# Performance work log

Hardware: AMD Instinct MI355X
Metric: run time of the kernel (lower is better)

The kernel has to match this reference:

```python
import jax, jax.numpy as jnp
import numpy as np
import math

B, N_AGENT, E = 32, 64, 256        # batch, agents, n_embd
DV, NV, HIS, DK = 32, 8, 50, 9     # head dim, heads, his_length, action_dim+1


def positional_encoding(max_seq_len, d_model):
    position = jnp.arange(max_seq_len, dtype=jnp.float32)[:, None]
    div_term = jnp.exp(jnp.arange(0, d_model, 2, dtype=jnp.float32) * (-math.log(10000.0) / d_model))
    pe = jnp.zeros((max_seq_len, d_model), jnp.float32)
    pe = pe.at[:, 0::2].set(jnp.sin(position * div_term))
    pe = pe.at[:, 1::2].set(jnp.cos(position * div_term))
    return pe


def setup_inputs() -> dict:
    key = jax.random.key(0)
    ks = jax.random.split(key, 12)
    q = jax.random.normal(ks[0], (B, N_AGENT, E), jnp.float32)
    k = jax.random.normal(ks[1], (B, HIS, N_AGENT, DK), jnp.float32)
    # adjacency: one-hot row selecting, per (agent, timestep), which agent's action to gather
    idx = jax.random.randint(ks[2], (N_AGENT, HIS), 0, N_AGENT)
    adjs_pos = jax.nn.one_hot(idx, N_AGENT, dtype=jnp.float32)  # [N, HIS, N]
    s = 0.05
    return {
        "q": q,
        "k": k,
        "adjs_pos": adjs_pos,
        "Wq": s * jax.random.normal(ks[3], (E, DV * NV), jnp.float32),
        "bq": jnp.zeros((DV * NV,), jnp.float32),
        "Wk": s * jax.random.normal(ks[4], (E, DV * NV), jnp.float32),
        "bk": jnp.zeros((DV * NV,), jnp.float32),
        "Wv": s * jax.random.normal(ks[5], (E, DV * NV), jnp.float32),
        "bv": jnp.zeros((DV * NV,), jnp.float32),
        "Wout": s * jax.random.normal(ks[6], (DV * NV, E), jnp.float32),
        "bout": jnp.zeros((E,), jnp.float32),
        "Wenc": s * jax.random.normal(ks[7], (DK, E), jnp.float32),
    }


def reference(q, k, adjs_pos, Wq, bq, Wk, bk, Wv, bv, Wout, bout, Wenc):
    b, n, e = q.shape
    d_k = k.shape[-1]  # torch code scales by sqrt(k.size(-1)) = 9
    pe = positional_encoding(HIS, e)  # [HIS, E]

    # query head: relu(Linear) then split heads -> [B, N, NV, DV]
    qh = jax.nn.relu(q @ Wq + bq).reshape(b, n, NV, DV)

    # adjacency gather: one-hot matmul selecting a neighbor's action per (agent, t)
    # avoids materializing the repeated [B,N,HIS,N,DK] tensor
    neigh = jnp.einsum('ntA,btAd->bntd', adjs_pos, k)  # [B, N, HIS, DK]

    # action encoder (GELU, exact erf as in nn.GELU) + positional encoding
    neigh = jax.nn.gelu(neigh @ Wenc, approximate=False) + pe  # [B, N, HIS, E]

    # key/value heads
    kh = jax.nn.relu(neigh @ Wk + bk).reshape(b, n, HIS, NV, DV)
    vh = jax.nn.relu(neigh @ Wv + bv).reshape(b, n, HIS, NV, DV)

    # attention over the history axis
    att = jnp.einsum('bnvd,bntvd->bnvt', qh, kh) / jnp.sqrt(jnp.float32(d_k))
    att = jax.nn.softmax(att, axis=-1)  # [B, N, NV, HIS]

    out = jnp.einsum('bnvt,bntvd->bnvd', att, vh).reshape(b, n, NV * DV)
    return jax.nn.relu(out @ Wout + bout)  # [B, N, E]
```

## Files before the change

### kernel.cpp

```cpp
#include <hip/hip_runtime.h>
#include <math.h>

#define NB   32
#define NA   64
#define EDIM 256
#define HIS  50
#define DKA  9
#define NV   8

typedef _Float16 HALF;
typedef _Float16 half4 __attribute__((ext_vector_type(4)));
typedef _Float16 half8 __attribute__((ext_vector_type(8)));
typedef float    f32x4 __attribute__((ext_vector_type(4)));

#define WS_WKP   0
#define WS_WVP   131072
#define WS_WQP   262144
#define WS_WOP   393216
#define WS_PEH   524288
#define WS_WET   549888
#define WS_IDX   566272
#define WS_QH    579072
#define WS_NEED  1627648ULL

__device__ __forceinline__ float gelu_exact(float x) {
    const float ax = fabsf(x) * 0.70710678118654752f;
    const float t  = __builtin_amdgcn_rcpf(1.0f + 0.3275911f * ax);
    const float p  = t * (0.254829592f + t * (-0.284496736f + t * (1.421413741f
                   + t * (-1.453152027f + t * 1.061405429f))));
    const float er = 1.0f - p * __expf(-ax * ax);
    return 0.5f * x * (1.0f + copysignf(er, x));
}

__global__ __launch_bounds__(256) void pack_setup(
    const float* __restrict__ Wk, const float* __restrict__ Wv,
    const float* __restrict__ Wq, const float* __restrict__ Wout,
    const float* __restrict__ adjs, const float* __restrict__ Wenc,
    char* __restrict__ ws)
{
    const int tid = blockIdx.x * 256 + threadIdx.x;
    HALF* WkP  = (HALF*)(ws + WS_WKP);
    HALF* WvP  = (HALF*)(ws + WS_WVP);
    HALF* WqP  = (HALF*)(ws + WS_WQP);
    HALF* WoP  = (HALF*)(ws + WS_WOP);
    HALF* PEH  = (HALF*)(ws + WS_PEH);
    HALF* WET  = (HALF*)(ws + WS_WET);
    int*  idxT = (int*)(ws + WS_IDX);

    {
        const int elem = tid & 7;
        const int lane = (tid >> 3) & 63;
        const int kt   = (tid >> 9) & 7;
        const int nt   = tid >> 12;
        const int k = kt * 32 + (lane >> 4) * 8 + elem;
        const int n = nt * 16 + (lane & 15);
        WkP[tid] = (HALF)Wk[k * EDIM + n];
        WvP[tid] = (HALF)Wv[k * EDIM + n];
        WqP[tid] = (HALF)Wq[k * EDIM + n];
        WoP[tid] = (HALF)Wout[k * EDIM + n];
    }
    if (tid < HIS * EDIM) {
        const int t = tid >> 8;
        const int e = tid & 255;
        const float dt = expf(-(float)(e & ~1) * (9.210340371976184f / 256.0f));
        const float arg = (float)t * dt;
        PEH[tid] = (HALF)((e & 1) ? cosf(arg) : sinf(arg));
    }
    if (tid < 16 * 64 * 8) {
        const int j    = tid & 7;
        const int lane = (tid >> 3) & 63;
        const int me   = tid >> 9;
        const int k = (lane >> 4) * 8 + j;
        const int e = me * 16 + (lane & 15);
        WET[tid] = (k < DKA) ? (HALF)Wenc[k * EDIM + e] : (HALF)0.0f;
    }
    if (tid < NA * HIS) {
        const float* row = adjs + tid * NA;
        int best = 0;
        #pragma unroll
        for (int a = 0; a < NA; ++a) best = (row[a] > 0.5f) ? a : best;
        idxT[tid] = best;
    }
}

__global__ __launch_bounds__(256) void qh_gemm(
    const float* __restrict__ q,
    const float* __restrict__ bq,
    const char*  __restrict__ ws,
    char* __restrict__ wsout)
{
    const int tid = threadIdx.x, lane = tid & 63, w = tid >> 6;
    const int l15 = lane & 15, l4 = lane >> 4;
    const int bx  = blockIdx.x;
    const int r0  = (bx >> 1) * 64;
    const int nh  = bx & 1;
    const HALF* WqP = (const HALF*)(ws + WS_WQP);
    HALF* qh = (HALF*)(wsout + WS_QH);

    f32x4 acc[4][2];
    #pragma unroll
    for (int mt = 0; mt < 4; ++mt)
        #pragma unroll
        for (int nt = 0; nt < 2; ++nt) acc[mt][nt] = (f32x4)0.0f;

    #pragma unroll 2
    for (int kk = 0; kk < 8; ++kk) {
        half8 afr[4];
        #pragma unroll
        for (int mt = 0; mt < 4; ++mt) {
            const float* ap = &q[(size_t)(r0 + mt * 16 + l15) * EDIM + kk * 32 + l4 * 8];
            const float4 a0 = *reinterpret_cast<const float4*>(ap);
            const float4 a1 = *reinterpret_cast<const float4*>(ap + 4);
            half8 h;
            h[0] = (HALF)a0.x; h[1] = (HALF)a0.y; h[2] = (HALF)a0.z; h[3] = (HALF)a0.w;
            h[4] = (HALF)a1.x; h[5] = (HALF)a1.y; h[6] = (HALF)a1.z; h[7] = (HALF)a1.w;
            afr[mt] = h;
        }
        #pragma unroll
        for (int nt = 0; nt < 2; ++nt) {
            const int ntile = nh * 8 + w * 2 + nt;
            const half8 bfr = *reinterpret_cast<const half8*>(
                WqP + ((size_t)(ntile * 8 + kk) * 64 + lane) * 8);
            #pragma unroll
            for (int mt = 0; mt < 4; ++mt)
                acc[mt][nt] = __builtin_amdgcn_mfma_f32_16x16x32_f16(afr[mt], bfr, acc[mt][nt], 0, 0, 0);
        }
    }

    #pragma unroll
    for (int nt = 0; nt < 2; ++nt) {
        const int col = (nh * 8 + w * 2 + nt) * 16 + l15;
        const float bqa = bq[col];
        #pragma unroll
        for (int mt = 0; mt < 4; ++mt)
            #pragma unroll
            for (int r = 0; r < 4; ++r) {
                const int row = l4 * 4 + r;
                qh[(size_t)(r0 + mt * 16 + row) * EDIM + col] =
                    (HALF)fmaxf(acc[mt][nt][r] + bqa, 0.0f);
            }
    }
}

__global__ __launch_bounds__(512, 4) void attn_fused(
    const float* __restrict__ kin,
    const float* __restrict__ bk,
    const float* __restrict__ bv,
    const char*  __restrict__ ws,
    char* __restrict__ wsout)
{
    const int tid  = threadIdx.x;
    const int lane = tid & 63;
    const int w    = tid >> 6;
    const int l15  = lane & 15;
    const int l4   = lane >> 4;
    const int bidx = blockIdx.x;
    const int b = bidx >> 6, n = bidx & 63;

    const HALF* WkP  = (const HALF*)(ws + WS_WKP);
    const HALF* WvP  = (const HALF*)(ws + WS_WVP);
    const HALF* PEH  = (const HALF*)(ws + WS_PEH);
    const HALF* WET  = (const HALF*)(ws + WS_WET);
    const HALF* qh   = (const HALF*)(ws + WS_QH);
    const int*  idxT = (const int*)(ws + WS_IDX);
    HALF* O = (HALF*)(wsout + WS_QH);

    __shared__ __align__(16) HALF  s_A[16384];
    __shared__ __align__(16) float s_un[1280];
    __shared__ float s_att[NV][64];

    HALF*  s_ng = (HALF*)s_un;
    float* s_o  = s_un;

    float qv[2], bkb[2], bvb[2];
    #pragma unroll
    for (int nt = 0; nt < 2; ++nt) {
        const int col = w * 32 + nt * 16 + l15;
        qv[nt]  = (float)qh[(size_t)bidx * EDIM + col];
        bkb[nt] = bk[col];
        bvb[nt] = bv[col];
    }

    #pragma unroll
    for (int i0 = 0; i0 < 64 * 32; i0 += 512) {
        const int i = i0 + tid;
        const int t = i >> 5;
        const int d = i & 31;
        float v = 0.0f;
        if (t < HIS && d < DKA)
            v = kin[((b * HIS + t) * NA + idxT[n * HIS + t]) * DKA + d];
        s_ng[t * 40 + d] = (HALF)v;
    }
    __syncthreads();

    {
        half8 aW[2];
        #pragma unroll
        for (int mi = 0; mi < 2; ++mi)
            aW[mi] = *reinterpret_cast<const half8*>(WET + ((size_t)(2 * w + mi) * 64 + lane) * 8);

        f32x4 accE[2][4];
        #pragma unroll
        for (int mi = 0; mi < 2; ++mi)
            #pragma unroll
            for (int nt = 0; nt < 4; ++nt) accE[mi][nt] = (f32x4)0.0f;

        #pragma unroll
        for (int nt = 0; nt < 4; ++nt) {
            const half8 bN = *reinterpret_cast<const half8*>(&s_ng[(nt * 16 + l15) * 40 + l4 * 8]);
            #pragma unroll
            for (int mi = 0; mi < 2; ++mi)
                accE[mi][nt] = __builtin_amdgcn_mfma_f32_16x16x32_f16(aW[mi], bN, accE[mi][nt], 0, 0, 0);
        }

        const int t_l = l4 & 1;
        #pragma unroll
        for (int mi = 0; mi < 2; ++mi) {
            const int me = 2 * w + mi;
            const int e0 = me * 16 + l4 * 4;
            const int fg = mi * 2 + (l4 >> 1);
            #pragma unroll
            for (int nt = 0; nt < 4; ++nt) {
                const int t = nt * 16 + l15;
                half4 hv;
                if (t < HIS) {
                    const half4 pe = *reinterpret_cast<const half4*>(PEH + t * EDIM + e0);
                    hv[0] = (HALF)(gelu_exact(accE[mi][nt][0]) + (float)pe[0]);
                    hv[1] = (HALF)(gelu_exact(accE[mi][nt][1]) + (float)pe[1]);
                    hv[2] = (HALF)(gelu_exact(accE[mi][nt][2]) + (float)pe[2]);
                    hv[3] = (HALF)(gelu_exact(accE[mi][nt][3]) + (float)pe[3]);
                } else {
                    hv[0] = (HALF)0.0f; hv[1] = (HALF)0.0f;
                    hv[2] = (HALF)0.0f; hv[3] = (HALF)0.0f;
                }
                const int gran = (w * 4 + nt) * 64 + ((fg * 16 + l15) ^ w);
                *reinterpret_cast<half4*>(&s_A[gran * 8 + t_l * 4]) = hv;
            }
        }
    }
    __syncthreads();

    f32x4 ka[4][2], va[4][2];
    #pragma unroll
    for (int mt = 0; mt < 4; ++mt)
        #pragma unroll
        for (int nt = 0; nt < 2; ++nt) { ka[mt][nt] = (f32x4)0.0f; va[mt][nt] = (f32x4)0.0f; }

    #pragma unroll
    for (int kk = 0; kk < 8; ++kk) {
        half8 afr[4];
        #pragma unroll
        for (int mt = 0; mt < 4; ++mt)
            afr[mt] = *reinterpret_cast<const half8*>(
                &s_A[((kk * 4 + mt) * 64 + (lane ^ kk)) * 8]);
        #pragma unroll
        for (int nt = 0; nt < 2; ++nt) {
            const size_t boff = ((size_t)((w * 2 + nt) * 8 + kk) * 64 + lane) * 8;
            const half8 bkfr = *reinterpret_cast<const half8*>(WkP + boff);
            const half8 bvfr = *reinterpret_cast<const half8*>(WvP + boff);
            #pragma unroll
            for (int mt = 0; mt < 4; ++mt) {
                ka[mt][nt] = __builtin_amdgcn_mfma_f32_16x16x32_f16(afr[mt], bkfr, ka[mt][nt], 0, 0, 0);
                va[mt][nt] = __builtin_amdgcn_mfma_f32_16x16x32_f16(afr[mt], bvfr, va[mt][nt], 0, 0, 0);
            }
        }
    }

    #pragma unroll
    for (int mt = 0; mt < 4; ++mt)
        #pragma unroll
        for (int r = 0; r < 4; ++r) {
            float p = qv[0] * fmaxf(ka[mt][0][r] + bkb[0], 0.0f)
                    + qv[1] * fmaxf(ka[mt][1][r] + bkb[1], 0.0f);
            p += __shfl_xor(p, 1);
            p += __shfl_xor(p, 2);
            p += __shfl_xor(p, 4);
            p += __shfl_xor(p, 8);
            if (l15 == 0) s_att[w][mt * 16 + l4 * 4 + r] = p * (1.0f / 3.0f);
        }

    {
        const float val = (lane < HIS) ? s_att[w][lane] : -1e30f;
        float m = val;
        m = fmaxf(m, __shfl_xor(m, 1));
        m = fmaxf(m, __shfl_xor(m, 2));
        m = fmaxf(m, __shfl_xor(m, 4));
        m = fmaxf(m, __shfl_xor(m, 8));
        m = fmaxf(m, __shfl_xor(m, 16));
        m = fmaxf(m, __shfl_xor(m, 32));
        const float e = (lane < HIS) ? __expf(val - m) : 0.0f;
        float s = e;
        s += __shfl_xor(s, 1);
        s += __shfl_xor(s, 2);
        s += __shfl_xor(s, 4);
        s += __shfl_xor(s, 8);
        s += __shfl_xor(s, 16);
        s += __shfl_xor(s, 32);
        s_att[w][lane] = e * __builtin_amdgcn_rcpf(s);
    }

    {
        float o0 = 0.f, o1 = 0.f;
        #pragma unroll
        for (int mt = 0; mt < 4; ++mt)
            #pragma unroll
            for (int r = 0; r < 4; ++r) {
                const int t = mt * 16 + l4 * 4 + r;
                const float a = s_att[w][t];
                o0 += a * fmaxf(va[mt][0][r] + bvb[0], 0.0f);
                o1 += a * fmaxf(va[mt][1][r] + bvb[1], 0.0f);
            }
        o0 += __shfl_xor(o0, 16); o1 += __shfl_xor(o1, 16);
        o0 += __shfl_xor(o0, 32); o1 += __shfl_xor(o1, 32);
        __syncthreads();
        if (lane < 16) {
            s_o[w * 32 +  0 + l15] = o0;
            s_o[w * 32 + 16 + l15] = o1;
        }
    }
    __syncthreads();

    if (tid < 256) O[(size_t)bidx * EDIM + tid] = (HALF)s_o[tid];
}

__global__ __launch_bounds__(256) void out_gemm(
    const float* __restrict__ bout,
    const char*  __restrict__ ws,
    float* __restrict__ out)
{
    const int tid = threadIdx.x, lane = tid & 63, w = tid >> 6;
    const int l15 = lane & 15, l4 = lane >> 4;
    const int bx  = blockIdx.x;
    const int r0  = (bx >> 1) * 64;
    const int nh  = bx & 1;
    const HALF* WoP = (const HALF*)(ws + WS_WOP);
    const HALF* O   = (const HALF*)(ws + WS_QH);

    f32x4 acc[4][2];
    #pragma unroll
    for (int mt = 0; mt < 4; ++mt)
        #pragma unroll
        for (int nt = 0; nt < 2; ++nt) acc[mt][nt] = (f32x4)0.0f;

    #pragma unroll 2
    for (int kk = 0; kk < 8; ++kk) {
        half8 afr[4];
        #pragma unroll
        for (int mt = 0; mt < 4; ++mt)
            afr[mt] = *reinterpret_cast<const half8*>(
                &O[(size_t)(r0 + mt * 16 + l15) * EDIM + kk * 32 + l4 * 8]);
        #pragma unroll
        for (int nt = 0; nt < 2; ++nt) {
            const int ntile = nh * 8 + w * 2 + nt;
            const half8 bfr = *reinterpret_cast<const half8*>(
                WoP + ((size_t)(ntile * 8 + kk) * 64 + lane) * 8);
            #pragma unroll
            for (int mt = 0; mt < 4; ++mt)
                acc[mt][nt] = __builtin_amdgcn_mfma_f32_16x16x32_f16(afr[mt], bfr, acc[mt][nt], 0, 0, 0);
        }
    }

    #pragma unroll
    for (int nt = 0; nt < 2; ++nt) {
        const int col = (nh * 8 + w * 2 + nt) * 16 + l15;
        const float boa = bout[col];
        #pragma unroll
        for (int mt = 0; mt < 4; ++mt)
            #pragma unroll
            for (int r = 0; r < 4; ++r) {
                const int row = l4 * 4 + r;
                out[(size_t)(r0 + mt * 16 + row) * EDIM + col] =
                    fmaxf(acc[mt][nt][r] + boa, 0.0f);
            }
    }
}

__global__ __launch_bounds__(256) void mha_fallback(
    const float* __restrict__ q,
    const float* __restrict__ kin,
    const float* __restrict__ adjs,
    const float* __restrict__ Wq, const float* __restrict__ bq,
    const float* __restrict__ Wk, const float* __restrict__ bk,
    const float* __restrict__ Wv, const float* __restrict__ bv,
    const float* __restrict__ Wout, const float* __restrict__ bout,
    const float* __restrict__ Wenc,
    float* __restrict__ out)
{
    const int tid  = threadIdx.x;
    const int bidx = blockIdx.x;
    const int b = bidx >> 6;
    const int n = bidx & 63;

    __shared__ __align__(16) float s_q[EDIM];
    __shared__ __align__(16) float s_qh[EDIM];
    __shared__ __align__(16) float s_neigh[HIS][12];
    __shared__ __align__(16) float s_enc[HIS * EDIM];
    __shared__ float s_att[NV][66];
    __shared__ __align__(16) float s_opart[4][EDIM];
    __shared__ __align__(16) float s_o[EDIM];
    __shared__ int s_idx[HIS];

    s_q[tid] = q[bidx * EDIM + tid];
    if (tid < HIS) {
        const float* row = adjs + (n * HIS + tid) * NA;
        int best = 0;
        #pragma unroll
        for (int a = 0; a < NA; ++a) best = (row[a] > 0.5f) ? a : best;
        s_idx[tid] = best;
    }
    __syncthreads();

    for (int i = tid; i < HIS * 12; i += 256) {
        const int t = i / 12;
        const int d = i - t * 12;
        float val = 0.0f;
        if (d < DKA) val = kin[((b * HIS + t) * NA + s_idx[t]) * DKA + d];
        s_neigh[t][d] = val;
    }
    __syncthreads();

    {
        const int e = tid;
        float acc = bq[e];
        #pragma unroll 4
        for (int d0 = 0; d0 < EDIM; d0 += 4) {
            const float4 qv = *reinterpret_cast<const float4*>(&s_q[d0]);
            acc += qv.x * Wq[(d0 + 0) * EDIM + e];
            acc += qv.y * Wq[(d0 + 1) * EDIM + e];
            acc += qv.z * Wq[(d0 + 2) * EDIM + e];
            acc += qv.w * Wq[(d0 + 3) * EDIM + e];
        }
        s_qh[e] = fmaxf(acc, 0.0f);

        float we[12];
        #pragma unroll
        for (int j = 0; j < 12; ++j) we[j] = (j < DKA) ? Wenc[j * EDIM + e] : 0.0f;
        const float dt = expf(-(float)(e & ~1) * (9.210340371976184f / 256.0f));
        for (int t = 0; t < HIS; ++t) {
            const float4 n0 = *reinterpret_cast<const float4*>(&s_neigh[t][0]);
            const float4 n1 = *reinterpret_cast<const float4*>(&s_neigh[t][4]);
            const float4 n2 = *reinterpret_cast<const float4*>(&s_neigh[t][8]);
            float x = n0.x*we[0] + n0.y*we[1] + n0.z*we[2] + n0.w*we[3]
                    + n1.x*we[4] + n1.y*we[5] + n1.z*we[6] + n1.w*we[7]
                    + n2.x*we[8];
            x = 0.5f * x * (1.0f + erff(x * 0.70710678118654752f));
            const float arg = (float)t * dt;
            const float pe = (e & 1) ? cosf(arg) : sinf(arg);
            s_enc[t * EDIM + e] = x + pe;
        }
    }
    __syncthreads();

    const int g = tid & 63;
    const int h = tid >> 6;
    const int tbase  = (h == 0) ? 0 : (h == 1) ? 13 : (h == 2) ? 25 : 37;
    const int tcount = (h == 1 || h == 2) ? 12 : 13;
    const int v = g >> 3;

    {
        float4 kacc[13];
        const float4 bkv = *reinterpret_cast<const float4*>(&bk[4 * g]);
        #pragma unroll
        for (int tt = 0; tt < 13; ++tt) kacc[tt] = bkv;
        #pragma unroll 2
        for (int d0 = 0; d0 < EDIM; d0 += 4) {
            const float4 w0 = *reinterpret_cast<const float4*>(&Wk[(d0 + 0) * EDIM + 4 * g]);
            const float4 w1 = *reinterpret_cast<const float4*>(&Wk[(d0 + 1) * EDIM + 4 * g]);
            const float4 w2 = *reinterpret_cast<const float4*>(&Wk[(d0 + 2) * EDIM + 4 * g]);
            const float4 w3 = *reinterpret_cast<const float4*>(&Wk[(d0 + 3) * EDIM + 4 * g]);
            #pragma unroll
            for (int tt = 0; tt < 13; ++tt) {
                const float4 ev = *reinterpret_cast<const float4*>(&s_enc[(tbase + tt) * EDIM + d0]);
                kacc[tt].x += ev.x * w0.x + ev.y * w1.x + ev.z * w2.x + ev.w * w3.x;
                kacc[tt].y += ev.x * w0.y + ev.y * w1.y + ev.z * w2.y + ev.w * w3.y;
                kacc[tt].z += ev.x * w0.z + ev.y * w1.z + ev.z * w2.z + ev.w * w3.z;
                kacc[tt].w += ev.x * w0.w + ev.y * w1.w + ev.z * w2.w + ev.w * w3.w;
            }
        }
        const float4 qv = *reinterpret_cast<const float4*>(&s_qh[4 * g]);
        #pragma unroll
        for (int tt = 0; tt < 13; ++tt) {
            float p = qv.x * fmaxf(kacc[tt].x, 0.0f)
                    + qv.y * fmaxf(kacc[tt].y, 0.0f)
                    + qv.z * fmaxf(kacc[tt].z, 0.0f)
                    + qv.w * fmaxf(kacc[tt].w, 0.0f);
            p += __shfl_xor(p, 1);
            p += __shfl_xor(p, 2);
            p += __shfl_xor(p, 4);
            if ((g & 7) == 0) s_att[v][tbase + tt] = p * (1.0f / 3.0f);
        }
    }
    __syncthreads();

    if (tid < NV) {
        float m = -1e30f;
        for (int t = 0; t < HIS; ++t) m = fmaxf(m, s_att[tid][t]);
        float ssum = 0.0f;
        for (int t = 0; t < HIS; ++t) {
            const float ex = expf(s_att[tid][t] - m);
            s_att[tid][t] = ex;
            ssum += ex;
        }
        const float inv = 1.0f / ssum;
        for (int t = 0; t < HIS; ++t) s_att[tid][t] *= inv;
    }
    __syncthreads();

    {
        float4 vacc[13];
        const float4 bvv = *reinterpret_cast<const float4*>(&bv[4 * g]);
        #pragma unroll
        for (int tt = 0; tt < 13; ++tt) vacc[tt] = bvv;
        #pragma unroll 2
        for (int d0 = 0; d0 < EDIM; d0 += 4) {
            const float4 w0 = *reinterpret_cast<const float4*>(&Wv[(d0 + 0) * EDIM + 4 * g]);
            const float4 w1 = *reinterpret_cast<const float4*>(&Wv[(d0 + 1) * EDIM + 4 * g]);
            const float4 w2 = *reinterpret_cast<const float4*>(&Wv[(d0 + 2) * EDIM + 4 * g]);
            const float4 w3 = *reinterpret_cast<const float4*>(&Wv[(d0 + 3) * EDIM + 4 * g]);
            #pragma unroll
            for (int tt = 0; tt < 13; ++tt) {
                const float4 ev = *reinterpret_cast<const float4*>(&s_enc[(tbase + tt) * EDIM + d0]);
                vacc[tt].x += ev.x * w0.x + ev.y * w1.x + ev.z * w2.x + ev.w * w3.x;
                vacc[tt].y += ev.x * w0.y + ev.y * w1.y + ev.z * w2.y + ev.w * w3.y;
                vacc[tt].z += ev.x * w0.z + ev.y * w1.z + ev.z * w2.z + ev.w * w3.z;
                vacc[tt].w += ev.x * w0.w + ev.y * w1.w + ev.z * w2.w + ev.w * w3.w;
            }
        }
        float4 po = make_float4(0.0f, 0.0f, 0.0f, 0.0f);
        #pragma unroll
        for (int tt = 0; tt < 13; ++tt) {
            if (tt < tcount) {
                const float a = s_att[v][tbase + tt];
                po.x += a * fmaxf(vacc[tt].x, 0.0f);
                po.y += a * fmaxf(vacc[tt].y, 0.0f);
                po.z += a * fmaxf(vacc[tt].z, 0.0f);
                po.w += a * fmaxf(vacc[tt].w, 0.0f);
            }
        }
        *reinterpret_cast<float4*>(&s_opart[h][4 * g]) = po;
    }
    __syncthreads();

    s_o[tid] = s_opart[0][tid] + s_opart[1][tid] + s_opart[2][tid] + s_opart[3][tid];
    __syncthreads();

    {
        const int e = tid;
        float acc = bout[e];
        #pragma unroll 4
        for (int d0 = 0; d0 < EDIM; d0 += 4) {
            const float4 ov = *reinterpret_cast<const float4*>(&s_o[d0]);
            acc += ov.x * Wout[(d0 + 0) * EDIM + e];
            acc += ov.y * Wout[(d0 + 1) * EDIM + e];
            acc += ov.z * Wout[(d0 + 2) * EDIM + e];
            acc += ov.w * Wout[(d0 + 3) * EDIM + e];
        }
        out[bidx * EDIM + e] = fmaxf(acc, 0.0f);
    }
}

extern "C" void kernel_launch(void* const* d_in, const int* in_sizes, int n_in,
                              void* d_out, int out_size, void* d_ws, size_t ws_size,
                              hipStream_t stream) {
    const float* q    = (const float*)d_in[0];
    const float* kin  = (const float*)d_in[1];
    const float* adjs = (const float*)d_in[2];
    const float* Wq   = (const float*)d_in[3];
    const float* bq   = (const float*)d_in[4];
    const float* Wk   = (const float*)d_in[5];
    const float* bk   = (const float*)d_in[6];
    const float* Wv   = (const float*)d_in[7];
    const float* bv   = (const float*)d_in[8];
    const float* Wout = (const float*)d_in[9];
    const float* bout = (const float*)d_in[10];
    const float* Wenc = (const float*)d_in[11];
    float* out = (float*)d_out;
    char* ws = (char*)d_ws;

    if (ws_size >= WS_NEED) {
        hipLaunchKernelGGL(pack_setup, dim3(256), dim3(256), 0, stream,
                           Wk, Wv, Wq, Wout, adjs, Wenc, ws);
        hipLaunchKernelGGL(qh_gemm, dim3(64), dim3(256), 0, stream,
                           q, bq, ws, ws);
        hipLaunchKernelGGL(attn_fused, dim3(NB * NA), dim3(512), 0, stream,
                           kin, bk, bv, ws, ws);
        hipLaunchKernelGGL(out_gemm, dim3(64), dim3(256), 0, stream,
                           bout, ws, out);
    } else {
        hipLaunchKernelGGL(mha_fallback, dim3(NB * NA), dim3(256), 0, stream,
                           q, kin, adjs, Wq, bq, Wk, bk, Wv, bv, Wout, bout, Wenc, out);
    }
}
```

Measured before the change: 82.60 us.

## Split K and V projections across waves, two rows per block

The attention kernel now handles two (batch, agent) rows per block with 1024 threads. Waves 0-7 compute the K projection and waves 8-15 compute the V projection, each over both rows, so every weight fragment loaded from global memory is reused for two rows. The Q and output GEMMs halve their row tile to 32 and double the grid to 128 blocks for better CU coverage. In exchange, shared memory per block doubles, block-wide syncs are added between the score, softmax and output phases, and occupancy may be limited by the 1024-thread blocks.

```diff
diff --git a/kernel.cpp b/kernel.cpp
--- a/kernel.cpp
+++ b/kernel.cpp
@@ -92,22 +92,22 @@
     const int tid = threadIdx.x, lane = tid & 63, w = tid >> 6;
     const int l15 = lane & 15, l4 = lane >> 4;
     const int bx  = blockIdx.x;
-    const int r0  = (bx >> 1) * 64;
+    const int r0  = (bx >> 1) * 32;
     const int nh  = bx & 1;
     const HALF* WqP = (const HALF*)(ws + WS_WQP);
     HALF* qh = (HALF*)(wsout + WS_QH);
 
-    f32x4 acc[4][2];
-    #pragma unroll
-    for (int mt = 0; mt < 4; ++mt)
+    f32x4 acc[2][2];
+    #pragma unroll
+    for (int mt = 0; mt < 2; ++mt)
         #pragma unroll
         for (int nt = 0; nt < 2; ++nt) acc[mt][nt] = (f32x4)0.0f;
 
     #pragma unroll 2
     for (int kk = 0; kk < 8; ++kk) {
-        half8 afr[4];
-        #pragma unroll
-        for (int mt = 0; mt < 4; ++mt) {
+        half8 afr[2];
+        #pragma unroll
+        for (int mt = 0; mt < 2; ++mt) {
             const float* ap = &q[(size_t)(r0 + mt * 16 + l15) * EDIM + kk * 32 + l4 * 8];
             const float4 a0 = *reinterpret_cast<const float4*>(ap);
             const float4 a1 = *reinterpret_cast<const float4*>(ap + 4);
@@ -122,7 +122,7 @@
             const half8 bfr = *reinterpret_cast<const half8*>(
                 WqP + ((size_t)(ntile * 8 + kk) * 64 + lane) * 8);
             #pragma unroll
-            for (int mt = 0; mt < 4; ++mt)
+            for (int mt = 0; mt < 2; ++mt)
                 acc[mt][nt] = __builtin_amdgcn_mfma_f32_16x16x32_f16(afr[mt], bfr, acc[mt][nt], 0, 0, 0);
         }
     }
@@ -132,7 +132,7 @@
         const int col = (nh * 8 + w * 2 + nt) * 16 + l15;
         const float bqa = bq[col];
         #pragma unroll
-        for (int mt = 0; mt < 4; ++mt)
+        for (int mt = 0; mt < 2; ++mt)
             #pragma unroll
             for (int r = 0; r < 4; ++r) {
                 const int row = l4 * 4 + r;
@@ -142,7 +142,7 @@
     }
 }
 
-__global__ __launch_bounds__(512, 4) void attn_fused(
+__global__ __launch_bounds__(1024, 4) void attn2(
     const float* __restrict__ kin,
     const float* __restrict__ bk,
     const float* __restrict__ bv,
@@ -152,10 +152,11 @@
     const int tid  = threadIdx.x;
     const int lane = tid & 63;
     const int w    = tid >> 6;
+    const int kv   = w >> 3;
+    const int hh   = w & 7;
     const int l15  = lane & 15;
     const int l4   = lane >> 4;
-    const int bidx = blockIdx.x;
-    const int b = bidx >> 6, n = bidx & 63;
+    const int bidx0 = blockIdx.x * 2;
 
     const HALF* WkP  = (const HALF*)(ws + WS_WKP);
     const HALF* WvP  = (const HALF*)(ws + WS_WVP);
@@ -165,39 +166,41 @@
     const int*  idxT = (const int*)(ws + WS_IDX);
     HALF* O = (HALF*)(wsout + WS_QH);
 
-    __shared__ __align__(16) HALF  s_A[16384];
-    __shared__ __align__(16) float s_un[1280];
-    __shared__ float s_att[NV][64];
-
-    HALF*  s_ng = (HALF*)s_un;
-    float* s_o  = s_un;
-
-    float qv[2], bkb[2], bvb[2];
+    __shared__ __align__(16) HALF  s_A[2 * 16384];
+    __shared__ __align__(16) HALF  s_ng[2 * 2560];
+    __shared__ float s_att[NV][2][64];
+    float* s_o = (float*)s_ng;
+
+    float qv[2][2], bb[2];
     #pragma unroll
     for (int nt = 0; nt < 2; ++nt) {
-        const int col = w * 32 + nt * 16 + l15;
-        qv[nt]  = (float)qh[(size_t)bidx * EDIM + col];
-        bkb[nt] = bk[col];
-        bvb[nt] = bv[col];
-    }
-
-    #pragma unroll
-    for (int i0 = 0; i0 < 64 * 32; i0 += 512) {
+        const int col = hh * 32 + nt * 16 + l15;
+        qv[0][nt] = (float)qh[(size_t)bidx0 * EDIM + col];
+        qv[1][nt] = (float)qh[(size_t)(bidx0 + 1) * EDIM + col];
+        bb[nt] = kv ? bv[col] : bk[col];
+    }
+
+    #pragma unroll
+    for (int i0 = 0; i0 < 2 * 64 * 32; i0 += 1024) {
         const int i = i0 + tid;
-        const int t = i >> 5;
+        const int g = i >> 11;
+        const int t = (i >> 5) & 63;
         const int d = i & 31;
         float v = 0.0f;
-        if (t < HIS && d < DKA)
-            v = kin[((b * HIS + t) * NA + idxT[n * HIS + t]) * DKA + d];
-        s_ng[t * 40 + d] = (HALF)v;
+        if (t < HIS && d < DKA) {
+            const int bidx = bidx0 + g;
+            v = kin[(((bidx >> 6) * HIS + t) * NA + idxT[(bidx & 63) * HIS + t]) * DKA + d];
+        }
+        s_ng[g * 2560 + t * 40 + d] = (HALF)v;
     }
     __syncthreads();
 
     {
+        const int g = kv;
         half8 aW[2];
         #pragma unroll
         for (int mi = 0; mi < 2; ++mi)
-            aW[mi] = *reinterpret_cast<const half8*>(WET + ((size_t)(2 * w + mi) * 64 + lane) * 8);
+            aW[mi] = *reinterpret_cast<const half8*>(WET + ((size_t)(2 * hh + mi) * 64 + lane) * 8);
 
         f32x4 accE[2][4];
         #pragma unroll
@@ -207,7 +210,8 @@
 
         #pragma unroll
         for (int nt = 0; nt < 4; ++nt) {
-            const half8 bN = *reinterpret_cast<const half8*>(&s_ng[(nt * 16 + l15) * 40 + l4 * 8]);
+            const half8 bN = *reinterpret_cast<const half8*>(
+                &s_ng[g * 2560 + (nt * 16 + l15) * 40 + l4 * 8]);
             #pragma unroll
             for (int mi = 0; mi < 2; ++mi)
                 accE[mi][nt] = __builtin_amdgcn_mfma_f32_16x16x32_f16(aW[mi], bN, accE[mi][nt], 0, 0, 0);
@@ -216,7 +220,7 @@
         const int t_l = l4 & 1;
         #pragma unroll
         for (int mi = 0; mi < 2; ++mi) {
-            const int me = 2 * w + mi;
+            const int me = 2 * hh + mi;
             const int e0 = me * 16 + l4 * 4;
             const int fg = mi * 2 + (l4 >> 1);
             #pragma unroll
@@ -233,54 +237,63 @@
                     hv[0] = (HALF)0.0f; hv[1] = (HALF)0.0f;
                     hv[2] = (HALF)0.0f; hv[3] = (HALF)0.0f;
                 }
-                const int gran = (w * 4 + nt) * 64 + ((fg * 16 + l15) ^ w);
-                *reinterpret_cast<half4*>(&s_A[gran * 8 + t_l * 4]) = hv;
+                const int gran = (hh * 4 + nt) * 64 + ((fg * 16 + l15) ^ hh);
+                *reinterpret_cast<half4*>(&s_A[g * 16384 + gran * 8 + t_l * 4]) = hv;
             }
         }
     }
     __syncthreads();
 
-    f32x4 ka[4][2], va[4][2];
-    #pragma unroll
-    for (int mt = 0; mt < 4; ++mt)
-        #pragma unroll
-        for (int nt = 0; nt < 2; ++nt) { ka[mt][nt] = (f32x4)0.0f; va[mt][nt] = (f32x4)0.0f; }
+    const HALF* BP = kv ? WvP : WkP;
+    f32x4 acc[2][4][2];
+    #pragma unroll
+    for (int g = 0; g < 2; ++g)
+        #pragma unroll
+        for (int mt = 0; mt < 4; ++mt)
+            #pragma unroll
+            for (int nt = 0; nt < 2; ++nt) acc[g][mt][nt] = (f32x4)0.0f;
 
     #pragma unroll
     for (int kk = 0; kk < 8; ++kk) {
-        half8 afr[4];
-        #pragma unroll
-        for (int mt = 0; mt < 4; ++mt)
-            afr[mt] = *reinterpret_cast<const half8*>(
-                &s_A[((kk * 4 + mt) * 64 + (lane ^ kk)) * 8]);
+        half8 afr[2][4];
+        #pragma unroll
+        for (int g = 0; g < 2; ++g)
+            #pragma unroll
+            for (int mt = 0; mt < 4; ++mt)
+                afr[g][mt] = *reinterpret_cast<const half8*>(
+                    &s_A[g * 16384 + ((kk * 4 + mt) * 64 + (lane ^ kk)) * 8]);
         #pragma unroll
         for (int nt = 0; nt < 2; ++nt) {
-            const size_t boff = ((size_t)((w * 2 + nt) * 8 + kk) * 64 + lane) * 8;
-            const half8 bkfr = *reinterpret_cast<const half8*>(WkP + boff);
-            const half8 bvfr = *reinterpret_cast<const half8*>(WvP + boff);
-            #pragma unroll
-            for (int mt = 0; mt < 4; ++mt) {
-                ka[mt][nt] = __builtin_amdgcn_mfma_f32_16x16x32_f16(afr[mt], bkfr, ka[mt][nt], 0, 0, 0);
-                va[mt][nt] = __builtin_amdgcn_mfma_f32_16x16x32_f16(afr[mt], bvfr, va[mt][nt], 0, 0, 0);
-            }
-        }
-    }
-
-    #pragma unroll
-    for (int mt = 0; mt < 4; ++mt)
-        #pragma unroll
-        for (int r = 0; r < 4; ++r) {
-            float p = qv[0] * fmaxf(ka[mt][0][r] + bkb[0], 0.0f)
-                    + qv[1] * fmaxf(ka[mt][1][r] + bkb[1], 0.0f);
-            p += __shfl_xor(p, 1);
-            p += __shfl_xor(p, 2);
-            p += __shfl_xor(p, 4);
-            p += __shfl_xor(p, 8);
-            if (l15 == 0) s_att[w][mt * 16 + l4 * 4 + r] = p * (1.0f / 3.0f);
-        }
+            const half8 bfr = *reinterpret_cast<const half8*>(
+                BP + (((hh * 2 + nt) * 8 + kk) * 64 + lane) * 8);
+            #pragma unroll
+            for (int g = 0; g < 2; ++g)
+                #pragma unroll
+                for (int mt = 0; mt < 4; ++mt)
+                    acc[g][mt][nt] = __builtin_amdgcn_mfma_f32_16x16x32_f16(afr[g][mt], bfr, acc[g][mt][nt], 0, 0, 0);
+        }
+    }
+
+    if (kv == 0) {
+        #pragma unroll
+        for (int g = 0; g < 2; ++g)
+            #pragma unroll
+            for (int mt = 0; mt < 4; ++mt)
+                #pragma unroll
+                for (int r = 0; r < 4; ++r) {
+                    float p = qv[g][0] * fmaxf(acc[g][mt][0][r] + bb[0], 0.0f)
+                            + qv[g][1] * fmaxf(acc[g][mt][1][r] + bb[1], 0.0f);
+                    p += __shfl_xor(p, 1);
+                    p += __shfl_xor(p, 2);
+                    p += __shfl_xor(p, 4);
+                    p += __shfl_xor(p, 8);
+                    if (l15 == 0) s_att[hh][g][mt * 16 + l4 * 4 + r] = p * (1.0f / 3.0f);
+                }
+    }
+    __syncthreads();
 
     {
-        const float val = (lane < HIS) ? s_att[w][lane] : -1e30f;
+        const float val = (lane < HIS) ? s_att[hh][kv][lane] : -1e30f;
         float m = val;
         m = fmaxf(m, __shfl_xor(m, 1));
         m = fmaxf(m, __shfl_xor(m, 2));
@@ -296,31 +309,38 @@
         s += __shfl_xor(s, 8);
         s += __shfl_xor(s, 16);
         s += __shfl_xor(s, 32);
-        s_att[w][lane] = e * __builtin_amdgcn_rcpf(s);
-    }
-
-    {
-        float o0 = 0.f, o1 = 0.f;
-        #pragma unroll
-        for (int mt = 0; mt < 4; ++mt)
-            #pragma unroll
-            for (int r = 0; r < 4; ++r) {
-                const int t = mt * 16 + l4 * 4 + r;
-                const float a = s_att[w][t];
-                o0 += a * fmaxf(va[mt][0][r] + bvb[0], 0.0f);
-                o1 += a * fmaxf(va[mt][1][r] + bvb[1], 0.0f);
+        s_att[hh][kv][lane] = e * __builtin_amdgcn_rcpf(s);
+    }
+    __syncthreads();
+
+    if (kv == 1) {
+        #pragma unroll
+        for (int g = 0; g < 2; ++g) {
+            float o0 = 0.f, o1 = 0.f;
+            #pragma unroll
+            for (int mt = 0; mt < 4; ++mt)
+                #pragma unroll
+                for (int r = 0; r < 4; ++r) {
+                    const int t = mt * 16 + l4 * 4 + r;
+                    const float a = s_att[hh][g][t];
+                    o0 += a * fmaxf(acc[g][mt][0][r] + bb[0], 0.0f);
+                    o1 += a * fmaxf(acc[g][mt][1][r] + bb[1], 0.0f);
+                }
+            o0 += __shfl_xor(o0, 16); o1 += __shfl_xor(o1, 16);
+            o0 += __shfl_xor(o0, 32); o1 += __shfl_xor(o1, 32);
+            if (lane < 16) {
+                s_o[g * 256 + hh * 32 +  0 + l15] = o0;
+                s_o[g * 256 + hh * 32 + 16 + l15] = o1;
             }
-        o0 += __shfl_xor(o0, 16); o1 += __shfl_xor(o1, 16);
-        o0 += __shfl_xor(o0, 32); o1 += __shfl_xor(o1, 32);
-        __syncthreads();
-        if (lane < 16) {
-            s_o[w * 32 +  0 + l15] = o0;
-            s_o[w * 32 + 16 + l15] = o1;
-        }
-    }
-    __syncthreads();
-
-    if (tid < 256) O[(size_t)bidx * EDIM + tid] = (HALF)s_o[tid];
+        }
+    }
+    __syncthreads();
+
+    if (tid < 512) {
+        const int g = tid >> 8;
+        const int c = tid & 255;
+        O[(size_t)(bidx0 + g) * EDIM + c] = (HALF)s_o[g * 256 + c];
+    }
 }
 
 __global__ __launch_bounds__(256) void out_gemm(
@@ -331,22 +351,22 @@
     const int tid = threadIdx.x, lane = tid & 63, w = tid >> 6;
     const int l15 = lane & 15, l4 = lane >> 4;
     const int bx  = blockIdx.x;
-    const int r0  = (bx >> 1) * 64;
+    const int r0  = (bx >> 1) * 32;
     const int nh  = bx & 1;
     const HALF* WoP = (const HALF*)(ws + WS_WOP);
     const HALF* O   = (const HALF*)(ws + WS_QH);
 
-    f32x4 acc[4][2];
-    #pragma unroll
-    for (int mt = 0; mt < 4; ++mt)
+    f32x4 acc[2][2];
+    #pragma unroll
+    for (int mt = 0; mt < 2; ++mt)
         #pragma unroll
         for (int nt = 0; nt < 2; ++nt) acc[mt][nt] = (f32x4)0.0f;
 
     #pragma unroll 2
     for (int kk = 0; kk < 8; ++kk) {
-        half8 afr[4];
-        #pragma unroll
-        for (int mt = 0; mt < 4; ++mt)
+        half8 afr[2];
+        #pragma unroll
+        for (int mt = 0; mt < 2; ++mt)
             afr[mt] = *reinterpret_cast<const half8*>(
                 &O[(size_t)(r0 + mt * 16 + l15) * EDIM + kk * 32 + l4 * 8]);
         #pragma unroll
@@ -355,7 +375,7 @@
             const half8 bfr = *reinterpret_cast<const half8*>(
                 WoP + ((size_t)(ntile * 8 + kk) * 64 + lane) * 8);
             #pragma unroll
-            for (int mt = 0; mt < 4; ++mt)
+            for (int mt = 0; mt < 2; ++mt)
                 acc[mt][nt] = __builtin_amdgcn_mfma_f32_16x16x32_f16(afr[mt], bfr, acc[mt][nt], 0, 0, 0);
         }
     }
@@ -365,7 +385,7 @@
         const int col = (nh * 8 + w * 2 + nt) * 16 + l15;
         const float boa = bout[col];
         #pragma unroll
-        for (int mt = 0; mt < 4; ++mt)
+        for (int mt = 0; mt < 2; ++mt)
             #pragma unroll
             for (int r = 0; r < 4; ++r) {
                 const int row = l4 * 4 + r;
@@ -580,11 +600,11 @@
     if (ws_size >= WS_NEED) {
         hipLaunchKernelGGL(pack_setup, dim3(256), dim3(256), 0, stream,
                            Wk, Wv, Wq, Wout, adjs, Wenc, ws);
-        hipLaunchKernelGGL(qh_gemm, dim3(64), dim3(256), 0, stream,
+        hipLaunchKernelGGL(qh_gemm, dim3(128), dim3(256), 0, stream,
                            q, bq, ws, ws);
-        hipLaunchKernelGGL(attn_fused, dim3(NB * NA), dim3(512), 0, stream,
+        hipLaunchKernelGGL(attn2, dim3(NB * NA / 2), dim3(1024), 0, stream,
                            kin, bk, bv, ws, ws);
-        hipLaunchKernelGGL(out_gemm, dim3(64), dim3(256), 0, stream,
+        hipLaunchKernelGGL(out_gemm, dim3(128), dim3(256), 0, stream,
                            bout, ws, out);
     } else {
         hipLaunchKernelGGL(mha_fallback, dim3(NB * NA), dim3(256), 0, stream,
```

Result: slower. 94.45 us (+14.3%).

## Process four (b,n) rows per attention block with double-buffered gather prefetch

Applied to the files above, without the earlier changes.

The attention kernel now handles four consecutive (batch, agent) rows per block. It hoists the Wenc fragment and bias loads out of the per-row loop and uses double-buffered shared memory, so the next row's neighbour gather is prefetched into registers while the current row's MFMA work runs. The qh and out GEMMs halve their row tile to 32 and double their grid to 128 blocks to spread work over more CUs. The attention grid shrinks to 512 blocks and shared memory roughly doubles (about 75 KB per block), which may lower occupancy and leave CUs idle.

```diff
diff --git a/kernel.cpp b/kernel.cpp
--- a/kernel.cpp
+++ b/kernel.cpp
@@ -92,22 +92,22 @@
     const int tid = threadIdx.x, lane = tid & 63, w = tid >> 6;
     const int l15 = lane & 15, l4 = lane >> 4;
     const int bx  = blockIdx.x;
-    const int r0  = (bx >> 1) * 64;
+    const int r0  = (bx >> 1) * 32;
     const int nh  = bx & 1;
     const HALF* WqP = (const HALF*)(ws + WS_WQP);
     HALF* qh = (HALF*)(wsout + WS_QH);
 
-    f32x4 acc[4][2];
+    f32x4 acc[2][2];
     #pragma unroll
-    for (int mt = 0; mt < 4; ++mt)
+    for (int mt = 0; mt < 2; ++mt)
         #pragma unroll
         for (int nt = 0; nt < 2; ++nt) acc[mt][nt] = (f32x4)0.0f;
 
     #pragma unroll 2
     for (int kk = 0; kk < 8; ++kk) {
-        half8 afr[4];
-        #pragma unroll
-        for (int mt = 0; mt < 4; ++mt) {
+        half8 afr[2];
+        #pragma unroll
+        for (int mt = 0; mt < 2; ++mt) {
             const float* ap = &q[(size_t)(r0 + mt * 16 + l15) * EDIM + kk * 32 + l4 * 8];
             const float4 a0 = *reinterpret_cast<const float4*>(ap);
             const float4 a1 = *reinterpret_cast<const float4*>(ap + 4);
@@ -122,7 +122,7 @@
             const half8 bfr = *reinterpret_cast<const half8*>(
                 WqP + ((size_t)(ntile * 8 + kk) * 64 + lane) * 8);
             #pragma unroll
-            for (int mt = 0; mt < 4; ++mt)
+            for (int mt = 0; mt < 2; ++mt)
                 acc[mt][nt] = __builtin_amdgcn_mfma_f32_16x16x32_f16(afr[mt], bfr, acc[mt][nt], 0, 0, 0);
         }
     }
@@ -132,7 +132,7 @@
         const int col = (nh * 8 + w * 2 + nt) * 16 + l15;
         const float bqa = bq[col];
         #pragma unroll
-        for (int mt = 0; mt < 4; ++mt)
+        for (int mt = 0; mt < 2; ++mt)
             #pragma unroll
             for (int r = 0; r < 4; ++r) {
                 const int row = l4 * 4 + r;
@@ -142,7 +142,7 @@
     }
 }
 
-__global__ __launch_bounds__(512, 4) void attn_fused(
+__global__ __launch_bounds__(512, 4) void attn3(
     const float* __restrict__ kin,
     const float* __restrict__ bk,
     const float* __restrict__ bv,
@@ -154,8 +154,6 @@
     const int w    = tid >> 6;
     const int l15  = lane & 15;
     const int l4   = lane >> 4;
-    const int bidx = blockIdx.x;
-    const int b = bidx >> 6, n = bidx & 63;
 
     const HALF* WkP  = (const HALF*)(ws + WS_WKP);
     const HALF* WvP  = (const HALF*)(ws + WS_WVP);
@@ -165,162 +163,199 @@
     const int*  idxT = (const int*)(ws + WS_IDX);
     HALF* O = (HALF*)(wsout + WS_QH);
 
-    __shared__ __align__(16) HALF  s_A[16384];
-    __shared__ __align__(16) float s_un[1280];
+    __shared__ __align__(16) HALF  s_A[2 * 16384];
+    __shared__ __align__(16) HALF  s_ng[2 * 2560];
     __shared__ float s_att[NV][64];
 
-    HALF*  s_ng = (HALF*)s_un;
-    float* s_o  = s_un;
-
-    float qv[2], bkb[2], bvb[2];
+    float bkb[2], bvb[2];
     #pragma unroll
     for (int nt = 0; nt < 2; ++nt) {
         const int col = w * 32 + nt * 16 + l15;
-        qv[nt]  = (float)qh[(size_t)bidx * EDIM + col];
         bkb[nt] = bk[col];
         bvb[nt] = bv[col];
     }
-
+    half8 aW[2];
     #pragma unroll
-    for (int i0 = 0; i0 < 64 * 32; i0 += 512) {
-        const int i = i0 + tid;
-        const int t = i >> 5;
-        const int d = i & 31;
-        float v = 0.0f;
-        if (t < HIS && d < DKA)
-            v = kin[((b * HIS + t) * NA + idxT[n * HIS + t]) * DKA + d];
-        s_ng[t * 40 + d] = (HALF)v;
-    }
-    __syncthreads();
+    for (int mi = 0; mi < 2; ++mi)
+        aW[mi] = *reinterpret_cast<const half8*>(WET + ((size_t)(2 * w + mi) * 64 + lane) * 8);
+
+    float gbuf[4];
 
     {
-        half8 aW[2];
-        #pragma unroll
-        for (int mi = 0; mi < 2; ++mi)
-            aW[mi] = *reinterpret_cast<const half8*>(WET + ((size_t)(2 * w + mi) * 64 + lane) * 8);
-
-        f32x4 accE[2][4];
-        #pragma unroll
-        for (int mi = 0; mi < 2; ++mi)
-            #pragma unroll
-            for (int nt = 0; nt < 4; ++nt) accE[mi][nt] = (f32x4)0.0f;
-
-        #pragma unroll
-        for (int nt = 0; nt < 4; ++nt) {
-            const half8 bN = *reinterpret_cast<const half8*>(&s_ng[(nt * 16 + l15) * 40 + l4 * 8]);
+        const int bidx = blockIdx.x * 4;
+        const int b = bidx >> 6, n = bidx & 63;
+        #pragma unroll
+        for (int s = 0; s < 4; ++s) {
+            const int i = s * 512 + tid;
+            const int t = i >> 5, d = i & 31;
+            float v = 0.0f;
+            if (t < HIS && d < DKA)
+                v = kin[((b * HIS + t) * NA + idxT[n * HIS + t]) * DKA + d];
+            gbuf[s] = v;
+        }
+        #pragma unroll
+        for (int s = 0; s < 4; ++s) {
+            const int i = s * 512 + tid;
+            s_ng[(i >> 5) * 40 + (i & 31)] = (HALF)gbuf[s];
+        }
+    }
+    __syncthreads();
+
+    for (int it = 0; it < 4; ++it) {
+        const int p = it & 1;
+        const int bidx = blockIdx.x * 4 + it;
+        HALF* sAp = s_A + p * 16384;
+
+        float qv[2];
+        #pragma unroll
+        for (int nt = 0; nt < 2; ++nt)
+            qv[nt] = (float)qh[(size_t)bidx * EDIM + w * 32 + nt * 16 + l15];
+
+        {
+            f32x4 accE[2][4];
             #pragma unroll
             for (int mi = 0; mi < 2; ++mi)
-                accE[mi][nt] = __builtin_amdgcn_mfma_f32_16x16x32_f16(aW[mi], bN, accE[mi][nt], 0, 0, 0);
-        }
-
-        const int t_l = l4 & 1;
-        #pragma unroll
-        for (int mi = 0; mi < 2; ++mi) {
-            const int me = 2 * w + mi;
-            const int e0 = me * 16 + l4 * 4;
-            const int fg = mi * 2 + (l4 >> 1);
+                #pragma unroll
+                for (int nt = 0; nt < 4; ++nt) accE[mi][nt] = (f32x4)0.0f;
+
             #pragma unroll
             for (int nt = 0; nt < 4; ++nt) {
-                const int t = nt * 16 + l15;
-                half4 hv;
-                if (t < HIS) {
-                    const half4 pe = *reinterpret_cast<const half4*>(PEH + t * EDIM + e0);
-                    hv[0] = (HALF)(gelu_exact(accE[mi][nt][0]) + (float)pe[0]);
-                    hv[1] = (HALF)(gelu_exact(accE[mi][nt][1]) + (float)pe[1]);
-                    hv[2] = (HALF)(gelu_exact(accE[mi][nt][2]) + (float)pe[2]);
-                    hv[3] = (HALF)(gelu_exact(accE[mi][nt][3]) + (float)pe[3]);
-                } else {
-                    hv[0] = (HALF)0.0f; hv[1] = (HALF)0.0f;
-                    hv[2] = (HALF)0.0f; hv[3] = (HALF)0.0f;
+                const half8 bN = *reinterpret_cast<const half8*>(
+                    &s_ng[p * 2560 + (nt * 16 + l15) * 40 + l4 * 8]);
+                #pragma unroll
+                for (int mi = 0; mi < 2; ++mi)
+                    accE[mi][nt] = __builtin_amdgcn_mfma_f32_16x16x32_f16(aW[mi], bN, accE[mi][nt], 0, 0, 0);
+            }
+
+            const int t_l = l4 & 1;
+            #pragma unroll
+            for (int mi = 0; mi < 2; ++mi) {
+                const int me = 2 * w + mi;
+                const int e0 = me * 16 + l4 * 4;
+                const int fg = mi * 2 + (l4 >> 1);
+                #pragma unroll
+                for (int nt = 0; nt < 4; ++nt) {
+                    const int t = nt * 16 + l15;
+                    half4 hv;
+                    if (t < HIS) {
+                        const half4 pe = *reinterpret_cast<const half4*>(PEH + t * EDIM + e0);
+                        hv[0] = (HALF)(gelu_exact(accE[mi][nt][0]) + (float)pe[0]);
+                        hv[1] = (HALF)(gelu_exact(accE[mi][nt][1]) + (float)pe[1]);
+                        hv[2] = (HALF)(gelu_exact(accE[mi][nt][2]) + (float)pe[2]);
+                        hv[3] = (HALF)(gelu_exact(accE[mi][nt][3]) + (float)pe[3]);
+                    } else {
+                        hv[0] = (HALF)0.0f; hv[1] = (HALF)0.0f;
+                        hv[2] = (HALF)0.0f; hv[3] = (HALF)0.0f;
+                    }
+                    const int gran = (w * 4 + nt) * 64 + ((fg * 16 + l15) ^ w);
+                    *reinterpret_cast<half4*>(&sAp[gran * 8 + t_l * 4]) = hv;
                 }
-                const int gran = (w * 4 + nt) * 64 + ((fg * 16 + l15) ^ w);
-                *reinterpret_cast<half4*>(&s_A[gran * 8 + t_l * 4]) = hv;
-            }
-        }
-    }
-    __syncthreads();
-
-    f32x4 ka[4][2], va[4][2];
-    #pragma unroll
-    for (int mt = 0; mt < 4; ++mt)
-        #pragma unroll
-        for (int nt = 0; nt < 2; ++nt) { ka[mt][nt] = (f32x4)0.0f; va[mt][nt] = (f32x4)0.0f; }
-
-    #pragma unroll
-    for (int kk = 0; kk < 8; ++kk) {
-        half8 afr[4];
+            }
+        }
+
+        if (it < 3) {
+            const int nb = bidx + 1;
+            const int b = nb >> 6, n = nb & 63;
+            #pragma unroll
+            for (int s = 0; s < 4; ++s) {
+                const int i = s * 512 + tid;
+                const int t = i >> 5, d = i & 31;
+                float v = 0.0f;
+                if (t < HIS && d < DKA)
+                    v = kin[((b * HIS + t) * NA + idxT[n * HIS + t]) * DKA + d];
+                gbuf[s] = v;
+            }
+        }
+
+        __syncthreads();
+
+        f32x4 ka[4][2], va[4][2];
         #pragma unroll
         for (int mt = 0; mt < 4; ++mt)
-            afr[mt] = *reinterpret_cast<const half8*>(
-                &s_A[((kk * 4 + mt) * 64 + (lane ^ kk)) * 8]);
-        #pragma unroll
-        for (int nt = 0; nt < 2; ++nt) {
-            const size_t boff = ((size_t)((w * 2 + nt) * 8 + kk) * 64 + lane) * 8;
-            const half8 bkfr = *reinterpret_cast<const half8*>(WkP + boff);
-            const half8 bvfr = *reinterpret_cast<const half8*>(WvP + boff);
-            #pragma unroll
-            for (int mt = 0; mt < 4; ++mt) {
-                ka[mt][nt] = __builtin_amdgcn_mfma_f32_16x16x32_f16(afr[mt], bkfr, ka[mt][nt], 0, 0, 0);
-                va[mt][nt] = __builtin_amdgcn_mfma_f32_16x16x32_f16(afr[mt], bvfr, va[mt][nt], 0, 0, 0);
-            }
-        }
-    }
-
-    #pragma unroll
-    for (int mt = 0; mt < 4; ++mt)
-        #pragma unroll
-        for (int r = 0; r < 4; ++r) {
-            float p = qv[0] * fmaxf(ka[mt][0][r] + bkb[0], 0.0f)
-                    + qv[1] * fmaxf(ka[mt][1][r] + bkb[1], 0.0f);
-            p += __shfl_xor(p, 1);
-            p += __shfl_xor(p, 2);
-            p += __shfl_xor(p, 4);
-            p += __shfl_xor(p, 8);
-            if (l15 == 0) s_att[w][mt * 16 + l4 * 4 + r] = p * (1.0f / 3.0f);
-        }
-
-    {
-        const float val = (lane < HIS) ? s_att[w][lane] : -1e30f;
-        float m = val;
-        m = fmaxf(m, __shfl_xor(m, 1));
-        m = fmaxf(m, __shfl_xor(m, 2));
-        m = fmaxf(m, __shfl_xor(m, 4));
-        m = fmaxf(m, __shfl_xor(m, 8));
-        m = fmaxf(m, __shfl_xor(m, 16));
-        m = fmaxf(m, __shfl_xor(m, 32));
-        const float e = (lane < HIS) ? __expf(val - m) : 0.0f;
-        float s = e;
-        s += __shfl_xor(s, 1);
-        s += __shfl_xor(s, 2);
-        s += __shfl_xor(s, 4);
-        s += __shfl_xor(s, 8);
-        s += __shfl_xor(s, 16);
-        s += __shfl_xor(s, 32);
-        s_att[w][lane] = e * __builtin_amdgcn_rcpf(s);
-    }
-
-    {
-        float o0 = 0.f, o1 = 0.f;
+            #pragma unroll
+            for (int nt = 0; nt < 2; ++nt) { ka[mt][nt] = (f32x4)0.0f; va[mt][nt] = (f32x4)0.0f; }
+
+        #pragma unroll
+        for (int kk = 0; kk < 8; ++kk) {
+            half8 afr[4];
+            #pragma unroll
+            for (int mt = 0; mt < 4; ++mt)
+                afr[mt] = *reinterpret_cast<const half8*>(
+                    &sAp[((kk * 4 + mt) * 64 + (lane ^ kk)) * 8]);
+            #pragma unroll
+            for (int nt = 0; nt < 2; ++nt) {
+                const size_t boff = ((size_t)((w * 2 + nt) * 8 + kk) * 64 + lane) * 8;
+                const half8 bkfr = *reinterpret_cast<const half8*>(WkP + boff);
+                const half8 bvfr = *reinterpret_cast<const half8*>(WvP + boff);
+                #pragma unroll
+                for (int mt = 0; mt < 4; ++mt) {
+                    ka[mt][nt] = __builtin_amdgcn_mfma_f32_16x16x32_f16(afr[mt], bkfr, ka[mt][nt], 0, 0, 0);
+                    va[mt][nt] = __builtin_amdgcn_mfma_f32_16x16x32_f16(afr[mt], bvfr, va[mt][nt], 0, 0, 0);
+                }
+            }
+        }
+
         #pragma unroll
         for (int mt = 0; mt < 4; ++mt)
             #pragma unroll
             for (int r = 0; r < 4; ++r) {
-                const int t = mt * 16 + l4 * 4 + r;
-                const float a = s_att[w][t];
-                o0 += a * fmaxf(va[mt][0][r] + bvb[0], 0.0f);
-                o1 += a * fmaxf(va[mt][1][r] + bvb[1], 0.0f);
-            }
-        o0 += __shfl_xor(o0, 16); o1 += __shfl_xor(o1, 16);
-        o0 += __shfl_xor(o0, 32); o1 += __shfl_xor(o1, 32);
+                float pp = qv[0] * fmaxf(ka[mt][0][r] + bkb[0], 0.0f)
+                         + qv[1] * fmaxf(ka[mt][1][r] + bkb[1], 0.0f);
+                pp += __shfl_xor(pp, 1);
+                pp += __shfl_xor(pp, 2);
+                pp += __shfl_xor(pp, 4);
+                pp += __shfl_xor(pp, 8);
+                if (l15 == 0) s_att[w][mt * 16 + l4 * 4 + r] = pp * (1.0f / 3.0f);
+            }
+
+        {
+            const float val = (lane < HIS) ? s_att[w][lane] : -1e30f;
+            float m = val;
+            m = fmaxf(m, __shfl_xor(m, 1));
+            m = fmaxf(m, __shfl_xor(m, 2));
+            m = fmaxf(m, __shfl_xor(m, 4));
+            m = fmaxf(m, __shfl_xor(m, 8));
+            m = fmaxf(m, __shfl_xor(m, 16));
+            m = fmaxf(m, __shfl_xor(m, 32));
+            const float e = (lane < HIS) ? __expf(val - m) : 0.0f;
+            float s = e;
+            s += __shfl_xor(s, 1);
+            s += __shfl_xor(s, 2);
+            s += __shfl_xor(s, 4);
+            s += __shfl_xor(s, 8);
+            s += __shfl_xor(s, 16);
+            s += __shfl_xor(s, 32);
+            s_att[w][lane] = e * __builtin_amdgcn_rcpf(s);
+        }
+
+        {
+            float o0 = 0.f, o1 = 0.f;
+            #pragma unroll
+            for (int mt = 0; mt < 4; ++mt)
+                #pragma unroll
+                for (int r = 0; r < 4; ++r) {
+                    const int t = mt * 16 + l4 * 4 + r;
+                    const float a = s_att[w][t];
+                    o0 += a * fmaxf(va[mt][0][r] + bvb[0], 0.0f);
+                    o1 += a * fmaxf(va[mt][1][r] + bvb[1], 0.0f);
+                }
+            o0 += __shfl_xor(o0, 16); o1 += __shfl_xor(o1, 16);
+            o0 += __shfl_xor(o0, 32); o1 += __shfl_xor(o1, 32);
+            if (lane < 16) {
+                O[(size_t)bidx * EDIM + w * 32 +  0 + l15] = (HALF)o0;
+                O[(size_t)bidx * EDIM + w * 32 + 16 + l15] = (HALF)o1;
+            }
+        }
+
+        if (it < 3) {
+            #pragma unroll
+            for (int s = 0; s < 4; ++s) {
+                const int i = s * 512 + tid;
+                s_ng[(p ^ 1) * 2560 + (i >> 5) * 40 + (i & 31)] = (HALF)gbuf[s];
+            }
+        }
         __syncthreads();
-        if (lane < 16) {
-            s_o[w * 32 +  0 + l15] = o0;
-            s_o[w * 32 + 16 + l15] = o1;
-        }
-    }
-    __syncthreads();
-
-    if (tid < 256) O[(size_t)bidx * EDIM + tid] = (HALF)s_o[tid];
+    }
 }
 
 __global__ __launch_bounds__(256) void out_gemm(
@@ -331,22 +366,22 @@
     const int tid = threadIdx.x, lane = tid & 63, w = tid >> 6;
     const int l15 = lane & 15, l4 = lane >> 4;
     const int bx  = blockIdx.x;
-    const int r0  = (bx >> 1) * 64;
+    const int r0  = (bx >> 1) * 32;
     const int nh  = bx & 1;
     const HALF* WoP = (const HALF*)(ws + WS_WOP);
     const HALF* O   = (const HALF*)(ws + WS_QH);
 
-    f32x4 acc[4][2];
+    f32x4 acc[2][2];
     #pragma unroll
-    for (int mt = 0; mt < 4; ++mt)
+    for (int mt = 0; mt < 2; ++mt)
         #pragma unroll
         for (int nt = 0; nt < 2; ++nt) acc[mt][nt] = (f32x4)0.0f;
 
     #pragma unroll 2
     for (int kk = 0; kk < 8; ++kk) {
-        half8 afr[4];
-        #pragma unroll
-        for (int mt = 0; mt < 4; ++mt)
+        half8 afr[2];
+        #pragma unroll
+        for (int mt = 0; mt < 2; ++mt)
             afr[mt] = *reinterpret_cast<const half8*>(
                 &O[(size_t)(r0 + mt * 16 + l15) * EDIM + kk * 32 + l4 * 8]);
         #pragma unroll
@@ -355,7 +390,7 @@
             const half8 bfr = *reinterpret_cast<const half8*>(
                 WoP + ((size_t)(ntile * 8 + kk) * 64 + lane) * 8);
             #pragma unroll
-            for (int mt = 0; mt < 4; ++mt)
+            for (int mt = 0; mt < 2; ++mt)
                 acc[mt][nt] = __builtin_amdgcn_mfma_f32_16x16x32_f16(afr[mt], bfr, acc[mt][nt], 0, 0, 0);
         }
     }
@@ -365,7 +400,7 @@
         const int col = (nh * 8 + w * 2 + nt) * 16 + l15;
         const float boa = bout[col];
         #pragma unroll
-        for (int mt = 0; mt < 4; ++mt)
+        for (int mt = 0; mt < 2; ++mt)
             #pragma unroll
             for (int r = 0; r < 4; ++r) {
                 const int row = l4 * 4 + r;
@@ -580,11 +615,11 @@
     if (ws_size >= WS_NEED) {
         hipLaunchKernelGGL(pack_setup, dim3(256), dim3(256), 0, stream,
                            Wk, Wv, Wq, Wout, adjs, Wenc, ws);
-        hipLaunchKernelGGL(qh_gemm, dim3(64), dim3(256), 0, stream,
+        hipLaunchKernelGGL(qh_gemm, dim3(128), dim3(256), 0, stream,
                            q, bq, ws, ws);
-        hipLaunchKernelGGL(attn_fused, dim3(NB * NA), dim3(512), 0, stream,
+        hipLaunchKernelGGL(attn3, dim3(NB * NA / 4), dim3(512), 0, stream,
                            kin, bk, bv, ws, ws);
-        hipLaunchKernelGGL(out_gemm, dim3(64), dim3(256), 0, stream,
+        hipLaunchKernelGGL(out_gemm, dim3(128), dim3(256), 0, stream,
                            bout, ws, out);
     } else {
         hipLaunchKernelGGL(mha_fallback, dim3(NB * NA), dim3(256), 0, stream,
```

New measurement: 182.2 us. 2.21x slower.
